# Kernel tuning notes

Measured on AMD Instinct MI355X. Metric: run time of the kernel, lower is better.

## Reference

```python
import jax, jax.numpy as jnp
import numpy as np

N_HEADS = 16
LN_EPS = 1e-5


def _rope(x, sin, cos):
    # Faithful to source: uses x.shape[0] (batch here) as 'length'.
    L = x.shape[0]
    x1, x2 = x[..., ::2], x[..., 1::2]
    c = cos[:L, None, :]  # broadcasts over dim 1 (seq)
    s = sin[:L, None, :]
    return jnp.concatenate([x1 * c - x2 * s, x1 * s + x2 * c], axis=-1)


def _layer_norm(x):
    m = jnp.mean(x, axis=-1, keepdims=True)
    v = jnp.var(x, axis=-1, keepdims=True)
    return (x - m) * jax.lax.rsqrt(v + LN_EPS)


def setup_inputs() -> dict:
    key = jax.random.key(0)
    ks = jax.random.split(key, 8)
    B, S, D = 2, 2048, 2048
    CTX = 2048
    x = jax.random.normal(ks[0], (B, S, D), dtype=jnp.float32)
    scale = 0.02
    Wq = jax.random.normal(ks[1], (D, D), dtype=jnp.float32) * scale
    Wk = jax.random.normal(ks[2], (D, D), dtype=jnp.float32) * scale
    Wv = jax.random.normal(ks[3], (D, D), dtype=jnp.float32) * scale
    W1 = jax.random.normal(ks[4], (D, 4 * D), dtype=jnp.float32) * scale
    b1 = jnp.zeros((4 * D,), dtype=jnp.float32)
    W2 = jax.random.normal(ks[5], (4 * D, D), dtype=jnp.float32) * scale
    b2 = jnp.zeros((D,), dtype=jnp.float32)
    inv_freq = 1.0 / (10000.0 ** (jnp.arange(0, D, 2, dtype=jnp.float32) / D))
    sinusoid = jnp.einsum('i,j->ij', jnp.arange(CTX, dtype=jnp.float32), inv_freq)
    sin = jnp.sin(sinusoid)
    cos = jnp.cos(sinusoid)
    return {"x": x, "Wq": Wq, "Wk": Wk, "Wv": Wv, "W1": W1, "b1": b1,
            "W2": W2, "b2": b2, "sin": sin, "cos": cos, "i": 0}


def reference(x, Wq, Wk, Wv, W1, b1, W2, b2, sin, cos, i):
    B, S, D = x.shape
    H = N_HEADS
    hd = D // H
    q = _rope(x @ Wq, sin, cos)
    k = _rope(x @ Wk, sin, cos)
    v = x @ Wv
    # [B,S,D] -> [B,H,S,hd]
    q = q.reshape(B, S, H, hd).transpose(0, 2, 1, 3)
    k = k.reshape(B, S, H, hd).transpose(0, 2, 1, 3)
    v = v.reshape(B, S, H, hd).transpose(0, 2, 1, 3)
    attn = jnp.einsum('bhqd,bhkd->bhqk', q, k) / jnp.sqrt(jnp.float32(hd))
    causal = jnp.tril(jnp.ones((S, S), dtype=bool))
    attn = jnp.where(causal[None, None], attn, -jnp.inf)
    attn = jax.nn.softmax(attn, axis=-1)
    out = jnp.einsum('bhqk,bhkd->bhqd', attn, v)
    out = out.transpose(0, 2, 1, 3).reshape(B, S, D)
    out = _layer_norm(out + x)
    h = jax.nn.gelu(out @ W1 + b1, approximate=False)
    out2 = _layer_norm(h @ W2 + b2 + out)
    return out2
```

## Files before the change

kernel.cpp:

```cpp
#include <hip/hip_runtime.h>
#include <hip/hip_bf16.h>
#include <math.h>
#include <stdint.h>

using bf16 = __hip_bfloat16;
typedef __attribute__((ext_vector_type(4))) float f32x4;
typedef __attribute__((ext_vector_type(8))) short s16x8;

#define MFMA16(a, b, c) __builtin_amdgcn_mfma_f32_16x16x32_bf16(a, b, c, 0, 0, 0)

__device__ __forceinline__ void gload_lds16(const void* g, void* l) {
    __builtin_amdgcn_global_load_lds(
        (const __attribute__((address_space(1))) void*)g,
        (__attribute__((address_space(3))) void*)l, 16, 0, 0);
}

struct alignas(16) bf16x8s { bf16 v[8]; };

__global__ void cvt_f32_bf16(const float* __restrict__ in, bf16* __restrict__ out, long n) {
    long i = ((long)blockIdx.x * 256 + threadIdx.x) * 8;
    if (i >= n) return;
    float4 a = *(const float4*)(in + i);
    float4 b = *(const float4*)(in + i + 4);
    bf16x8s r;
    r.v[0] = __float2bfloat16(a.x); r.v[1] = __float2bfloat16(a.y);
    r.v[2] = __float2bfloat16(a.z); r.v[3] = __float2bfloat16(a.w);
    r.v[4] = __float2bfloat16(b.x); r.v[5] = __float2bfloat16(b.y);
    r.v[6] = __float2bfloat16(b.z); r.v[7] = __float2bfloat16(b.w);
    *(bf16x8s*)(out + i) = r;
}

__global__ void transpose_cvt(const float* __restrict__ W, bf16* __restrict__ Wt, int K, int N) {
    __shared__ bf16 t[32][33];
    int tx = threadIdx.x & 31, ty = threadIdx.x >> 5;
    int n0 = blockIdx.x * 32, k0 = blockIdx.y * 32;
    #pragma unroll
    for (int r = ty; r < 32; r += 8)
        t[r][tx] = __float2bfloat16(W[(size_t)(k0 + r) * N + n0 + tx]);
    __syncthreads();
    #pragma unroll
    for (int r = ty; r < 32; r += 8)
        Wt[(size_t)(n0 + r) * K + k0 + tx] = t[tx][r];
}

#define GEMM_LDS 131072

template <int EPI, int SPLITK>
__global__ __launch_bounds__(512) void gemm_pipe(
    const bf16* __restrict__ A, const bf16* __restrict__ Bt,
    void* __restrict__ C, const float* __restrict__ bias,
    const float* __restrict__ resid, int M, int N, int K)
{
    __shared__ __align__(16) char smem[GEMM_LDS];
    const int tid = threadIdx.x;
    const int wid = tid >> 6, lane = tid & 63;
    const int quad = lane >> 4, l16 = lane & 15;
    const int wm = wid >> 2, wn = wid & 3;

    const int nx = gridDim.x;
    const int nwg = nx * gridDim.y;
    int lin = blockIdx.y * nx + blockIdx.x;
    const int cpx = nwg >> 3;
    lin = (lin & 7) * cpx + (lin >> 3);
    const int bm = (lin % nx) * 256, bn = (lin / nx) * 256;

    const int KH = K / SPLITK;
    const int kbeg = blockIdx.z * KH;
    const int NT = KH / 64;

    const int r0 = tid >> 3, pb = tid & 7;
    const int gcol = ((pb ^ (r0 & 7)) << 3);
    const bf16* pA[2][2];
    const bf16* pB[2][2];
    #pragma unroll
    for (int h = 0; h < 2; ++h)
        #pragma unroll
        for (int j = 0; j < 2; ++j) {
            pA[h][j] = A + (size_t)(bm + h * 64 + j * 128 + r0) * K + kbeg + gcol;
            pB[h][j] = Bt + (size_t)(bn + ((r0 >> 5) + 2 * j) * 64 + h * 32 + (r0 & 31)) * K
                       + kbeg + gcol;
        }
    const int dA0 = tid * 16;
    const int dA1 = 16384 + tid * 16;
    const int dB0 = 32768 + tid * 16;
    const int dB1 = 49152 + tid * 16;

#define ST_A(h, base, T1) { \
    gload_lds16(pA[h][0] + (T1) * 64, smem + (base)); \
    gload_lds16(pA[h][1] + (T1) * 64, smem + (base) + 8192); }
#define ST_B(h, base, T1) { \
    gload_lds16(pB[h][0] + (T1) * 64, smem + (base)); \
    gload_lds16(pB[h][1] + (T1) * 64, smem + (base) + 8192); }

    const int asw = l16 & 7;
    const int kx0 = (quad ^ asw) << 3;
    const int kx1 = ((4 + quad) ^ asw) << 3;
    const int aq0 = wm * 4096 + l16 * 64;
    const int aq1 = (2 + wm) * 4096 + l16 * 64;
    const int bq0 = 16384 + wn * 2048 + l16 * 64;
    const int bq1 = bq0 + 8192;

#define LDA(base) { _Pragma("unroll") for (int mt = 0; mt < 4; ++mt) { \
    aF[0][mt] = *(const s16x8*)(sa + (base) + mt * 1024 + kx0); \
    aF[1][mt] = *(const s16x8*)(sa + (base) + mt * 1024 + kx1); } }
#define LDB(base) { _Pragma("unroll") for (int nt = 0; nt < 2; ++nt) { \
    bF[0][nt] = *(const s16x8*)(sa + (base) + nt * 1024 + kx0); \
    bF[1][nt] = *(const s16x8*)(sa + (base) + nt * 1024 + kx1); } }
#define MM(mo, no) { \
    __builtin_amdgcn_s_setprio(1); \
    _Pragma("unroll") for (int kh = 0; kh < 2; ++kh) \
    _Pragma("unroll") for (int mt = 0; mt < 4; ++mt) \
    _Pragma("unroll") for (int nt = 0; nt < 2; ++nt) \
        acc[(mo) + mt][(no) + nt] = MFMA16(aF[kh][mt], bF[kh][nt], acc[(mo) + mt][(no) + nt]); \
    __builtin_amdgcn_s_setprio(0); }

    f32x4 acc[8][4] = {};
    s16x8 aF[2][4], bF[2][2];

    ST_A(0, dA0, 0); ST_B(0, dB0, 0);
    ST_A(1, dA1, 0);
    ST_B(1, dB1, 0);
    asm volatile("s_waitcnt vmcnt(4)" ::: "memory");
    __builtin_amdgcn_s_barrier();

    for (int t = 0; t < NT - 1; ++t) {
        const int sl = t & 1;
        const bf16* sa = (const bf16*)smem + sl * 32768;
        const int sb1 = (sl ^ 1) * 65536;
        LDA(aq0); LDB(bq0);
        ST_A(0, sb1 + dA0, t + 1); ST_B(0, sb1 + dB0, t + 1);
        MM(0, 0);
        asm volatile("s_waitcnt vmcnt(6)" ::: "memory");
        __builtin_amdgcn_s_barrier();
        LDA(aq1);
        ST_A(1, sb1 + dA1, t + 1);
        MM(4, 0);
        asm volatile("s_waitcnt vmcnt(6)" ::: "memory");
        __builtin_amdgcn_s_barrier();
        LDB(bq1);
        ST_B(1, sb1 + dB1, t + 1);
        MM(4, 2);
        LDA(aq0);
        MM(0, 2);
        asm volatile("s_waitcnt vmcnt(4)" ::: "memory");
        __builtin_amdgcn_s_barrier();
    }
    {
        const bf16* sa = (const bf16*)smem + ((NT - 1) & 1) * 32768;
        LDA(aq0); LDB(bq0);
        MM(0, 0);
        asm volatile("s_waitcnt vmcnt(2)" ::: "memory");
        __builtin_amdgcn_s_barrier();
        LDA(aq1);
        MM(4, 0);
        asm volatile("s_waitcnt vmcnt(0)" ::: "memory");
        __builtin_amdgcn_s_barrier();
        LDB(bq1);
        MM(4, 2);
        LDA(aq0);
        MM(0, 2);
    }
#undef ST_A
#undef ST_B
#undef LDA
#undef LDB
#undef MM

    float* Cp = (float*)C;
    if (EPI == 3) Cp += (size_t)blockIdx.z * M * N;

    #pragma unroll
    for (int m = 0; m < 8; ++m) {
        #pragma unroll
        for (int n = 0; n < 4; ++n) {
            #pragma unroll
            for (int r = 0; r < 4; ++r) {
                int row = bm + wm * 128 + m * 16 + quad * 4 + r;
                int col = bn + wn * 64 + n * 16 + l16;
                float v = acc[m][n][r];
                if (EPI == 0) {
                    ((bf16*)C)[(size_t)row * N + col] = __float2bfloat16(v);
                } else if (EPI == 1) {
                    float xx = v + bias[col];
                    float g = 0.5f * xx * (1.0f + erff(xx * 0.7071067811865475f));
                    ((bf16*)C)[(size_t)row * N + col] = __float2bfloat16(g);
                } else if (EPI == 2) {
                    ((float*)C)[(size_t)row * N + col] =
                        v + bias[col] + resid[(size_t)row * N + col];
                } else {
                    Cp[(size_t)row * N + col] = v;
                }
            }
        }
    }
}

__global__ void rope_kernel(const bf16* __restrict__ in, bf16* __restrict__ out,
                            const float* __restrict__ sn, const float* __restrict__ cs,
                            int S, int D, int instride) {
    int row = blockIdx.x;
    int pos = row / S;
    const int half = D >> 1;
    const bf16* r = in + (size_t)row * instride;
    bf16* o = out + (size_t)row * D;
    for (int j = threadIdx.x; j < half; j += 256) {
        uint32_t pr = *(const uint32_t*)(r + 2 * j);
        float x1 = __uint_as_float(pr << 16);
        float x2 = __uint_as_float(pr & 0xffff0000u);
        float c = cs[(size_t)pos * half + j], s = sn[(size_t)pos * half + j];
        o[j]        = __float2bfloat16(x1 * c - x2 * s);
        o[half + j] = __float2bfloat16(x1 * s + x2 * c);
    }
}

__global__ void vtrans_kernel(const bf16* __restrict__ v, bf16* __restrict__ vt,
                              int S, int D, int H, int instride) {
    __shared__ bf16 t[32][33];
    int bh = blockIdx.z, b = bh >> 4, h = bh & 15;
    int s0 = blockIdx.x * 32, d0 = blockIdx.y * 32;
    int tx = threadIdx.x & 31, ty = threadIdx.x >> 5;
    #pragma unroll
    for (int r = ty; r < 32; r += 8)
        t[r][tx] = v[(size_t)(b * S + s0 + r) * instride + h * 128 + d0 + tx];
    __syncthreads();
    #pragma unroll
    for (int r = ty; r < 32; r += 8)
        vt[((size_t)bh * 128 + d0 + r) * S + s0 + tx] = t[tx][r];
}

__global__ __launch_bounds__(256, 4) void attn_kernel(
    const bf16* __restrict__ q, const bf16* __restrict__ k, const bf16* __restrict__ vt,
    float* __restrict__ o, int S, int D, int H)
{
    __shared__ __align__(16) char smem[40960];
    bf16* Ks = (bf16*)smem;
    bf16* Vs = (bf16*)(smem + 16384);
    bf16* Ps = (bf16*)(smem + 32768);

    const int tid = threadIdx.x, wid = tid >> 6, lane = tid & 63;
    const int quad = lane >> 4, l16 = lane & 15;
    const int bh = blockIdx.x, b = bh >> 4, h = bh & 15;
    const int qt = gridDim.y - 1 - blockIdx.y;
    const float scale = 0.08838834764831845f;

    s16x8 qf[4];
    const bf16* qrow = q + ((size_t)(b * S + qt * 64 + wid * 16 + l16)) * D + h * 128;
    #pragma unroll
    for (int ks = 0; ks < 4; ++ks)
        qf[ks] = *(const s16x8*)(qrow + ks * 32 + quad * 8);

    f32x4 oacc[8] = {};
    float mstate = -INFINITY, lstate = 0.f;

    const bf16* kb0 = k + (size_t)(b * S) * D + h * 128;
    const bf16* vb0 = vt + (size_t)bh * 128 * S;
    bf16* psw = Ps + wid * 16 * 64;
    const int sw = l16 & 7;
    const int nch = qt + 1;

    for (int kc = 0; kc < nch; ++kc) {
        __syncthreads();
        #pragma unroll
        for (int c = 0; c < 4; ++c) {
            int choff = (wid * 4 + c) << 10;
            int off = choff + lane * 16;
            int rk = off >> 8, bk = (off & 255) >> 4;
            gload_lds16(kb0 + (size_t)(kc * 64 + rk) * D + ((bk ^ (rk & 7)) << 3),
                        (char*)Ks + choff);
            int rv = off >> 7, bv = (off & 127) >> 4;
            gload_lds16(vb0 + (size_t)rv * S + kc * 64 + ((bv ^ (rv & 7)) << 3),
                        (char*)Vs + choff);
        }
        __syncthreads();

        f32x4 sacc[4] = {};
        #pragma unroll
        for (int mt = 0; mt < 4; ++mt) {
            #pragma unroll
            for (int ks = 0; ks < 4; ++ks) {
                s16x8 kf = *(const s16x8*)(Ks + (mt * 16 + l16) * 128 +
                                           (((ks * 4 + quad) ^ sw) << 3));
                sacc[mt] = MFMA16(kf, qf[ks], sacc[mt]);
            }
        }

        const bool need_mask = (kc == qt);
        #pragma unroll
        for (int mt = 0; mt < 4; ++mt)
            #pragma unroll
            for (int r = 0; r < 4; ++r) {
                float vv = sacc[mt][r] * scale;
                if (need_mask) {
                    int kl = mt * 16 + quad * 4 + r;
                    if (kl > wid * 16 + l16) vv = -INFINITY;
                }
                sacc[mt][r] = vv;
            }

        float mx = fmaxf(fmaxf(fmaxf(sacc[0][0], sacc[0][1]), fmaxf(sacc[0][2], sacc[0][3])),
                         fmaxf(fmaxf(sacc[1][0], sacc[1][1]), fmaxf(sacc[1][2], sacc[1][3])));
        mx = fmaxf(mx, fmaxf(fmaxf(fmaxf(sacc[2][0], sacc[2][1]), fmaxf(sacc[2][2], sacc[2][3])),
                             fmaxf(fmaxf(sacc[3][0], sacc[3][1]), fmaxf(sacc[3][2], sacc[3][3]))));
        mx = fmaxf(mx, __shfl_xor(mx, 16, 64));
        mx = fmaxf(mx, __shfl_xor(mx, 32, 64));
        float mnew = fmaxf(mstate, mx);
        float alpha = __expf(mstate - mnew);
        float rs = 0.f;
        #pragma unroll
        for (int mt = 0; mt < 4; ++mt)
            #pragma unroll
            for (int r = 0; r < 4; ++r) {
                float p = __expf(sacc[mt][r] - mnew);
                sacc[mt][r] = p;
                rs += p;
            }
        rs += __shfl_xor(rs, 16, 64);
        rs += __shfl_xor(rs, 32, 64);
        lstate = lstate * alpha + rs;
        mstate = mnew;
        #pragma unroll
        for (int mt = 0; mt < 8; ++mt)
            #pragma unroll
            for (int r = 0; r < 4; ++r) oacc[mt][r] *= alpha;

        #pragma unroll
        for (int mt = 0; mt < 4; ++mt)
            #pragma unroll
            for (int r = 0; r < 4; ++r) {
                int kl = mt * 16 + quad * 4 + r;
                psw[l16 * 64 + (((kl >> 3) ^ sw) << 3) + (kl & 7)] =
                    __float2bfloat16(sacc[mt][r]);
            }

        #pragma unroll
        for (int ks2 = 0; ks2 < 2; ++ks2) {
            s16x8 pf = *(const s16x8*)(psw + l16 * 64 + (((ks2 * 4 + quad) ^ sw) << 3));
            #pragma unroll
            for (int mt = 0; mt < 8; ++mt) {
                s16x8 vf = *(const s16x8*)(Vs + (mt * 16 + l16) * 64 +
                                           (((ks2 * 4 + quad) ^ sw) << 3));
                oacc[mt] = MFMA16(vf, pf, oacc[mt]);
            }
        }
    }

    float inv = 1.0f / lstate;
    __syncthreads();
    float* osw = (float*)smem + wid * 16 * 130;
    #pragma unroll
    for (int mt = 0; mt < 8; ++mt)
        #pragma unroll
        for (int r = 0; r < 4; ++r)
            osw[l16 * 130 + mt * 16 + quad * 4 + r] = oacc[mt][r] * inv;
    float* obase = o + (size_t)(b * S + qt * 64 + wid * 16) * D + h * 128;
    #pragma unroll
    for (int r16 = 0; r16 < 16; ++r16) {
        float2 val = *(const float2*)(osw + r16 * 130 + lane * 2);
        *(float2*)(obase + (size_t)r16 * D + lane * 2) = val;
    }
}

__global__ __launch_bounds__(256) void ln_kernel(
    const float* __restrict__ a, const float* __restrict__ b,
    const float* __restrict__ c, const float* __restrict__ bias,
    float* __restrict__ outf, bf16* __restrict__ outb, int D)
{
    int row = blockIdx.x;
    const float* pa = a + (size_t)row * D;
    const float* pb = b ? b + (size_t)row * D : nullptr;
    const float* pc = c ? c + (size_t)row * D : nullptr;
    float v[8];
    float sum = 0.f, sq = 0.f;
    #pragma unroll
    for (int u = 0; u < 8; ++u) {
        int j = threadIdx.x + u * 256;
        float x = pa[j];
        if (pb) x += pb[j];
        if (pc) x += pc[j];
        if (bias) x += bias[j];
        v[u] = x; sum += x; sq += x * x;
    }
    #pragma unroll
    for (int off = 32; off > 0; off >>= 1) {
        sum += __shfl_down(sum, off, 64);
        sq  += __shfl_down(sq,  off, 64);
    }
    __shared__ float red[8];
    int wid = threadIdx.x >> 6, lane = threadIdx.x & 63;
    if (lane == 0) { red[wid] = sum; red[4 + wid] = sq; }
    __syncthreads();
    sum = red[0] + red[1] + red[2] + red[3];
    sq  = red[4] + red[5] + red[6] + red[7];
    float mean = sum / D;
    float var = sq / D - mean * mean;
    float rstd = rsqrtf(fmaxf(var, 0.f) + 1e-5f);
    float* pof = outf ? outf + (size_t)row * D : nullptr;
    bf16* pob = outb ? outb + (size_t)row * D : nullptr;
    #pragma unroll
    for (int u = 0; u < 8; ++u) {
        int j = threadIdx.x + u * 256;
        float y = (v[u] - mean) * rstd;
        if (pof) pof[j] = y;
        if (pob) pob[j] = __float2bfloat16(y);
    }
}

extern "C" void kernel_launch(void* const* d_in, const int* in_sizes, int n_in,
                              void* d_out, int out_size, void* d_ws, size_t ws_size,
                              hipStream_t stream) {
    const float* x  = (const float*)d_in[0];
    const float* Wq = (const float*)d_in[1];
    const float* Wk = (const float*)d_in[2];
    const float* Wv = (const float*)d_in[3];
    const float* W1 = (const float*)d_in[4];
    const float* b1 = (const float*)d_in[5];
    const float* W2 = (const float*)d_in[6];
    const float* b2 = (const float*)d_in[7];
    const float* sn = (const float*)d_in[8];
    const float* cs = (const float*)d_in[9];

    const int B = 2, S = 2048, D = 2048, H = 16, Dff = 8192;
    const int M = B * S;
    const int NQKV = 3 * D;
    char* ws = (char*)d_ws;
    const size_t MB = 1024 * 1024;

    const size_t o_xb   = 0;
    const size_t o_Wqkv = 16 * MB;
    const size_t o_qkv  = 40 * MB;
    const size_t o_qr   = 0;
    const size_t o_kr   = 16 * MB;
    const size_t o_vt   = 88 * MB;
    const size_t o_attn = 40 * MB;
    const size_t o_outb = 0;
    const size_t o_outf = 72 * MB;
    const size_t o_W1t  = 16 * MB;
    const size_t o_h    = 104 * MB;
    const size_t o_W2t  = 16 * MB;
    const size_t o_p    = 168 * MB;

    long nx = (long)M * D;
    cvt_f32_bf16<<<nx / 2048, 256, 0, stream>>>(x, (bf16*)(ws + o_xb), nx);
    transpose_cvt<<<dim3(D / 32, D / 32), 256, 0, stream>>>(
        Wq, (bf16*)(ws + o_Wqkv), D, D);
    transpose_cvt<<<dim3(D / 32, D / 32), 256, 0, stream>>>(
        Wk, (bf16*)(ws + o_Wqkv) + (size_t)D * D, D, D);
    transpose_cvt<<<dim3(D / 32, D / 32), 256, 0, stream>>>(
        Wv, (bf16*)(ws + o_Wqkv) + 2 * (size_t)D * D, D, D);

    gemm_pipe<0, 1><<<dim3(M / 256, NQKV / 256), 512, 0, stream>>>(
        (bf16*)(ws + o_xb), (bf16*)(ws + o_Wqkv), ws + o_qkv, nullptr, nullptr,
        M, NQKV, D);

    rope_kernel<<<M, 256, 0, stream>>>((bf16*)(ws + o_qkv), (bf16*)(ws + o_qr),
                                       sn, cs, S, D, NQKV);
    rope_kernel<<<M, 256, 0, stream>>>((bf16*)(ws + o_qkv) + D, (bf16*)(ws + o_kr),
                                       sn, cs, S, D, NQKV);
    vtrans_kernel<<<dim3(S / 32, 4, B * H), 256, 0, stream>>>(
        (bf16*)(ws + o_qkv) + 2 * D, (bf16*)(ws + o_vt), S, D, H, NQKV);

    attn_kernel<<<dim3(B * H, S / 64), 256, 0, stream>>>(
        (bf16*)(ws + o_qr), (bf16*)(ws + o_kr), (bf16*)(ws + o_vt),
        (float*)(ws + o_attn), S, D, H);

    ln_kernel<<<M, 256, 0, stream>>>((float*)(ws + o_attn), x, nullptr, nullptr,
                                     (float*)(ws + o_outf), (bf16*)(ws + o_outb), D);

    transpose_cvt<<<dim3(Dff / 32, D / 32), 256, 0, stream>>>(
        W1, (bf16*)(ws + o_W1t), D, Dff);
    gemm_pipe<1, 1><<<dim3(M / 256, Dff / 256), 512, 0, stream>>>(
        (bf16*)(ws + o_outb), (bf16*)(ws + o_W1t), ws + o_h, b1, nullptr, M, Dff, D);

    transpose_cvt<<<dim3(D / 32, Dff / 32), 256, 0, stream>>>(
        W2, (bf16*)(ws + o_W2t), Dff, D);
    gemm_pipe<3, 2><<<dim3(M / 256, D / 256, 2), 512, 0, stream>>>(
        (bf16*)(ws + o_h), (bf16*)(ws + o_W2t), ws + o_p, nullptr, nullptr, M, D, Dff);

    ln_kernel<<<M, 256, 0, stream>>>((float*)(ws + o_p),
                                     (float*)(ws + o_p) + (size_t)M * D,
                                     (float*)(ws + o_outf), b2,
                                     (float*)d_out, nullptr, D);
}
```

Measured before the change: 781.5 us.

## Double-buffer GEMM register fragments to overlap LDS reads with MFMA

Restructures the GEMM main loop so that A/B fragments are held in two register sets (fA0/fA1, fB0/fB1). The next tile's first fragments are loaded from LDS during the current tile's last MFMA block, and the per-iteration barriers drop from three to two. Global-to-LDS address pointers are now computed from one base with offsets instead of a precomputed pointer array. The aim is to hide LDS read latency and cut synchronisation, at the cost of more VGPRs and a possible occupancy or spill risk.

```diff
diff --git a/kernel.cpp b/kernel.cpp
--- a/kernel.cpp
+++ b/kernel.cpp
@@ -43,15 +43,13 @@
         Wt[(size_t)(n0 + r) * K + k0 + tx] = t[tx][r];
 }
 
-#define GEMM_LDS 131072
-
 template <int EPI, int SPLITK>
 __global__ __launch_bounds__(512) void gemm_pipe(
     const bf16* __restrict__ A, const bf16* __restrict__ Bt,
     void* __restrict__ C, const float* __restrict__ bias,
     const float* __restrict__ resid, int M, int N, int K)
 {
-    __shared__ __align__(16) char smem[GEMM_LDS];
+    __shared__ __align__(16) char smem[131072];
     const int tid = threadIdx.x;
     const int wid = tid >> 6, lane = tid & 63;
     const int quad = lane >> 4, l16 = lane & 15;
@@ -70,100 +68,79 @@
 
     const int r0 = tid >> 3, pb = tid & 7;
     const int gcol = ((pb ^ (r0 & 7)) << 3);
-    const bf16* pA[2][2];
-    const bf16* pB[2][2];
-    #pragma unroll
-    for (int h = 0; h < 2; ++h)
-        #pragma unroll
-        for (int j = 0; j < 2; ++j) {
-            pA[h][j] = A + (size_t)(bm + h * 64 + j * 128 + r0) * K + kbeg + gcol;
-            pB[h][j] = Bt + (size_t)(bn + ((r0 >> 5) + 2 * j) * 64 + h * 32 + (r0 & 31)) * K
-                       + kbeg + gcol;
-        }
-    const int dA0 = tid * 16;
-    const int dA1 = 16384 + tid * 16;
-    const int dB0 = 32768 + tid * 16;
-    const int dB1 = 49152 + tid * 16;
-
-#define ST_A(h, base, T1) { \
-    gload_lds16(pA[h][0] + (T1) * 64, smem + (base)); \
-    gload_lds16(pA[h][1] + (T1) * 64, smem + (base) + 8192); }
-#define ST_B(h, base, T1) { \
-    gload_lds16(pB[h][0] + (T1) * 64, smem + (base)); \
-    gload_lds16(pB[h][1] + (T1) * 64, smem + (base) + 8192); }
+    const bf16* pA00 = A + (size_t)(bm + r0) * K + kbeg + gcol;
+    const bf16* pB00 = Bt + (size_t)(bn + (r0 >> 5) * 64 + (r0 & 31)) * K + kbeg + gcol;
+    const int dA = tid * 16;
+    const int dB = 32768 + tid * 16;
+
+#define ST_A(h, sb, T1) { \
+    gload_lds16(pA00 + (size_t)((h) * 64      ) * K + (T1) * 64, smem + (sb) + (h) * 16384 + dA); \
+    gload_lds16(pA00 + (size_t)((h) * 64 + 128) * K + (T1) * 64, smem + (sb) + (h) * 16384 + dA + 8192); }
+#define ST_B(h, sb, T1) { \
+    gload_lds16(pB00 + (size_t)((h) * 32      ) * K + (T1) * 64, smem + (sb) + (h) * 16384 + dB); \
+    gload_lds16(pB00 + (size_t)((h) * 32 + 128) * K + (T1) * 64, smem + (sb) + (h) * 16384 + dB + 8192); }
 
     const int asw = l16 & 7;
     const int kx0 = (quad ^ asw) << 3;
     const int kx1 = ((4 + quad) ^ asw) << 3;
     const int aq0 = wm * 4096 + l16 * 64;
-    const int aq1 = (2 + wm) * 4096 + l16 * 64;
+    const int aq1 = 8192 + wm * 4096 + l16 * 64;
     const int bq0 = 16384 + wn * 2048 + l16 * 64;
     const int bq1 = bq0 + 8192;
-
-#define LDA(base) { _Pragma("unroll") for (int mt = 0; mt < 4; ++mt) { \
-    aF[0][mt] = *(const s16x8*)(sa + (base) + mt * 1024 + kx0); \
-    aF[1][mt] = *(const s16x8*)(sa + (base) + mt * 1024 + kx1); } }
-#define LDB(base) { _Pragma("unroll") for (int nt = 0; nt < 2; ++nt) { \
-    bF[0][nt] = *(const s16x8*)(sa + (base) + nt * 1024 + kx0); \
-    bF[1][nt] = *(const s16x8*)(sa + (base) + nt * 1024 + kx1); } }
-#define MM(mo, no) { \
+    const bf16* sm = (const bf16*)smem;
+
+#define LD_A(dst, off) { _Pragma("unroll") for (int mt = 0; mt < 4; ++mt) { \
+    dst[0][mt] = *(const s16x8*)(sm + (off) + mt * 1024 + kx0); \
+    dst[1][mt] = *(const s16x8*)(sm + (off) + mt * 1024 + kx1); } }
+#define LD_B(dst, off) { _Pragma("unroll") for (int nt = 0; nt < 2; ++nt) { \
+    dst[0][nt] = *(const s16x8*)(sm + (off) + nt * 1024 + kx0); \
+    dst[1][nt] = *(const s16x8*)(sm + (off) + nt * 1024 + kx1); } }
+#define MM(fa, fb, mo, no) { \
     __builtin_amdgcn_s_setprio(1); \
     _Pragma("unroll") for (int kh = 0; kh < 2; ++kh) \
     _Pragma("unroll") for (int mt = 0; mt < 4; ++mt) \
     _Pragma("unroll") for (int nt = 0; nt < 2; ++nt) \
-        acc[(mo) + mt][(no) + nt] = MFMA16(aF[kh][mt], bF[kh][nt], acc[(mo) + mt][(no) + nt]); \
+        acc[(mo) + mt][(no) + nt] = MFMA16(fa[kh][mt], fb[kh][nt], acc[(mo) + mt][(no) + nt]); \
     __builtin_amdgcn_s_setprio(0); }
 
     f32x4 acc[8][4] = {};
-    s16x8 aF[2][4], bF[2][2];
-
-    ST_A(0, dA0, 0); ST_B(0, dB0, 0);
-    ST_A(1, dA1, 0);
-    ST_B(1, dB1, 0);
-    asm volatile("s_waitcnt vmcnt(4)" ::: "memory");
-    __builtin_amdgcn_s_barrier();
+    s16x8 fA0[2][4], fA1[2][4], fB0[2][2], fB1[2][2];
+
+    ST_A(0, 0, 0); ST_B(0, 0, 0); ST_A(1, 0, 0);
+    ST_B(1, 0, 0);
+    asm volatile("s_waitcnt vmcnt(2)\ns_barrier" ::: "memory");
+    LD_A(fA0, aq0); LD_B(fB0, bq0);
 
     for (int t = 0; t < NT - 1; ++t) {
-        const int sl = t & 1;
-        const bf16* sa = (const bf16*)smem + sl * 32768;
-        const int sb1 = (sl ^ 1) * 65536;
-        LDA(aq0); LDB(bq0);
-        ST_A(0, sb1 + dA0, t + 1); ST_B(0, sb1 + dB0, t + 1);
-        MM(0, 0);
-        asm volatile("s_waitcnt vmcnt(6)" ::: "memory");
-        __builtin_amdgcn_s_barrier();
-        LDA(aq1);
-        ST_A(1, sb1 + dA1, t + 1);
-        MM(4, 0);
-        asm volatile("s_waitcnt vmcnt(6)" ::: "memory");
-        __builtin_amdgcn_s_barrier();
-        LDB(bq1);
-        ST_B(1, sb1 + dB1, t + 1);
-        MM(4, 2);
-        LDA(aq0);
-        MM(0, 2);
-        asm volatile("s_waitcnt vmcnt(4)" ::: "memory");
-        __builtin_amdgcn_s_barrier();
+        const int ce = (t & 1) << 15;
+        const int ne = ce ^ 32768;
+        const int nb = ne << 1;
+        LD_A(fA1, ce + aq1);
+        ST_A(0, nb, t + 1); ST_B(0, nb, t + 1); ST_A(1, nb, t + 1);
+        MM(fA0, fB0, 0, 0);
+        asm volatile("s_waitcnt vmcnt(6)\ns_barrier" ::: "memory");
+        LD_B(fB1, ce + bq1);
+        ST_B(1, nb, t + 1);
+        MM(fA1, fB0, 4, 0);
+        MM(fA0, fB1, 0, 2);
+        asm volatile("s_waitcnt vmcnt(2)\ns_barrier" ::: "memory");
+        LD_A(fA0, ne + aq0); LD_B(fB0, ne + bq0);
+        MM(fA1, fB1, 4, 2);
     }
     {
-        const bf16* sa = (const bf16*)smem + ((NT - 1) & 1) * 32768;
-        LDA(aq0); LDB(bq0);
-        MM(0, 0);
-        asm volatile("s_waitcnt vmcnt(2)" ::: "memory");
-        __builtin_amdgcn_s_barrier();
-        LDA(aq1);
-        MM(4, 0);
-        asm volatile("s_waitcnt vmcnt(0)" ::: "memory");
-        __builtin_amdgcn_s_barrier();
-        LDB(bq1);
-        MM(4, 2);
-        LDA(aq0);
-        MM(0, 2);
+        const int ce = ((NT - 1) & 1) << 15;
+        LD_A(fA1, ce + aq1);
+        MM(fA0, fB0, 0, 0);
+        asm volatile("s_waitcnt vmcnt(0)\ns_barrier" ::: "memory");
+        LD_B(fB1, ce + bq1);
+        MM(fA1, fB0, 4, 0);
+        MM(fA0, fB1, 0, 2);
+        MM(fA1, fB1, 4, 2);
     }
 #undef ST_A
 #undef ST_B
-#undef LDA
-#undef LDB
+#undef LD_A
+#undef LD_B
 #undef MM
 
     float* Cp = (float*)C;
```

Result: slower. 797.6 us (+2.1%).
